# Optimization experiments

Measured on AMD Instinct MI355X. Metric: run time of the kernel, lower is better.

Reference implementation:

```python
import jax, jax.numpy as jnp
from jax import lax
import numpy as np

T, B, NIN, H, NOUT = 256, 64, 512, 512, 512


def _lstm_dir(x, w_ih, w_hh, b_ih, b_hh, reverse):
    # x: [T,B,NIN]; w_ih: [4H,NIN]; w_hh: [4H,H]
    xg = jnp.einsum('tbi,gi->tbg', x, w_ih) + b_ih + b_hh  # [T,B,4H]
    if reverse:
        xg = xg[::-1]
    h0 = jnp.zeros((x.shape[1], w_hh.shape[1]), x.dtype)

    def step(carry, g):
        h, c = carry
        g = g + h @ w_hh.T
        i, f, gg, o = jnp.split(g, 4, axis=-1)  # PyTorch gate order i,f,g,o
        i = jax.nn.sigmoid(i)
        f = jax.nn.sigmoid(f)
        gg = jnp.tanh(gg)
        o = jax.nn.sigmoid(o)
        c = f * c + i * gg
        h = o * jnp.tanh(c)
        return (h, c), h

    _, hs = lax.scan(step, (h0, h0), xg)
    if reverse:
        hs = hs[::-1]
    return hs  # [T,B,H]


def setup_inputs() -> dict:
    key = jax.random.key(0)
    ks = jax.random.split(key, 12)
    s_in = 1.0 / np.sqrt(H)
    u = lambda k, shape: jax.random.uniform(k, shape, jnp.float32, -s_in, s_in)
    return {
        'x': jax.random.normal(ks[0], (T, B, NIN), jnp.float32),
        'w_ih_f': u(ks[1], (4 * H, NIN)),
        'w_hh_f': u(ks[2], (4 * H, H)),
        'b_ih_f': u(ks[3], (4 * H,)),
        'b_hh_f': u(ks[4], (4 * H,)),
        'w_ih_b': u(ks[5], (4 * H, NIN)),
        'w_hh_b': u(ks[6], (4 * H, H)),
        'b_ih_b': u(ks[7], (4 * H,)),
        'b_hh_b': u(ks[8], (4 * H,)),
        'fc_w': u(ks[9], (NOUT, 2 * H)),
        'fc_b': u(ks[10], (NOUT,)),
    }


def reference(x, w_ih_f, w_hh_f, b_ih_f, b_hh_f, w_ih_b, w_hh_b, b_ih_b, b_hh_b, fc_w, fc_b):
    h_f = _lstm_dir(x, w_ih_f, w_hh_f, b_ih_f, b_hh_f, reverse=False)
    h_b = _lstm_dir(x, w_ih_b, w_hh_b, b_ih_b, b_hh_b, reverse=True)
    h = jnp.concatenate([h_f, h_b], axis=-1)  # [T,B,2H]
    out = jnp.einsum('tbh,oh->tbo', h, fc_w) + fc_b  # fused linear over T*B rows
    return out
```

## Files before the change

kernel.cpp:

```cpp
#include <hip/hip_runtime.h>

typedef unsigned short u16;
typedef short v8s __attribute__((ext_vector_type(8)));
typedef float v4f __attribute__((ext_vector_type(4)));

#define TT 256
#define BB 64
#define HH 512
#define G4 2048
#define MTB 16384

static __device__ __forceinline__ float bf2f(u16 u) {
    unsigned int x = ((unsigned int)u) << 16;
    union { unsigned int i; float f; } c; c.i = x; return c.f;
}
static __device__ __forceinline__ u16 f2bf(float f) {
    union { float f; unsigned int i; } c; c.f = f;
    unsigned int u = c.i;
    u += 0x7fffu + ((u >> 16) & 1u);
    return (u16)(u >> 16);
}

__global__ __launch_bounds__(256) void cvt_bf16(const float* __restrict__ src,
                                                u16* __restrict__ dst, int n) {
    int i = blockIdx.x * blockDim.x + threadIdx.x;
    int stride = gridDim.x * blockDim.x;
    for (int j = i * 4; j < n; j += stride * 4) {
        float4 v = *reinterpret_cast<const float4*>(src + j);
        ushort4 o;
        o.x = f2bf(v.x); o.y = f2bf(v.y); o.z = f2bf(v.z); o.w = f2bf(v.w);
        *reinterpret_cast<ushort4*>(dst + j) = o;
    }
}

template<bool OUT_BF16, bool BIAS_M>
__global__ __launch_bounds__(256) void gemm_bt(const u16* __restrict__ A,
                                               const u16* __restrict__ Bm,
                                               void* __restrict__ Cv,
                                               const float* __restrict__ bias1,
                                               const float* __restrict__ bias2,
                                               int M, int N, int K) {
    __shared__ u16 lds_a[128 * 64];
    __shared__ u16 lds_b[128 * 64];
    const int tid = threadIdx.x, lane = tid & 63;
    const int m0 = blockIdx.y * 128, n0 = blockIdx.x * 128;
    const int wid = tid >> 6, wm = wid >> 1, wn = wid & 1;
    v4f acc[4][4] = {};

    const int srow  = tid >> 3;
    const int skoff = (tid & 7) * 8;
    const u16* Ag = A + (size_t)(m0 + srow) * K + skoff;
    const u16* Bg = Bm + (size_t)(n0 + srow) * K + skoff;
    u16* la = lds_a + srow * 64 + skoff;
    u16* lb = lds_b + srow * 64 + skoff;

    for (int k0 = 0; k0 < K; k0 += 64) {
        #pragma unroll
        for (int q = 0; q < 4; ++q) {
            *reinterpret_cast<v8s*>(la + q * 32 * 64) =
                *reinterpret_cast<const v8s*>(Ag + (size_t)q * 32 * K + k0);
            *reinterpret_cast<v8s*>(lb + q * 32 * 64) =
                *reinterpret_cast<const v8s*>(Bg + (size_t)q * 32 * K + k0);
        }
        __syncthreads();
        #pragma unroll
        for (int kk = 0; kk < 2; ++kk) {
            v8s af[4], bfr[4];
            #pragma unroll
            for (int i = 0; i < 4; ++i)
                af[i] = *reinterpret_cast<const v8s*>(
                    lds_a + (wm * 64 + i * 16 + (lane & 15)) * 64 + kk * 32 + (lane >> 4) * 8);
            #pragma unroll
            for (int i = 0; i < 4; ++i)
                bfr[i] = *reinterpret_cast<const v8s*>(
                    lds_b + (wn * 64 + i * 16 + (lane & 15)) * 64 + kk * 32 + (lane >> 4) * 8);
            #pragma unroll
            for (int i = 0; i < 4; ++i)
                #pragma unroll
                for (int j = 0; j < 4; ++j)
                    acc[i][j] = __builtin_amdgcn_mfma_f32_16x16x32_bf16(af[i], bfr[j], acc[i][j], 0, 0, 0);
        }
        __syncthreads();
    }
    #pragma unroll
    for (int i = 0; i < 4; ++i) {
        #pragma unroll
        for (int j = 0; j < 4; ++j) {
            #pragma unroll
            for (int r = 0; r < 4; ++r) {
                int m = m0 + wm * 64 + i * 16 + (lane >> 4) * 4 + r;
                int n = n0 + wn * 64 + j * 16 + (lane & 15);
                float v = acc[i][j][r];
                if (BIAS_M) { v += bias1[m]; if (bias2) v += bias2[m]; }
                else        { v += bias1[n]; }
                if (OUT_BF16) ((u16*)Cv)[(size_t)m * N + n] = f2bf(v);
                else          ((float*)Cv)[(size_t)m * N + n] = v;
            }
        }
    }
}

static __device__ __forceinline__ float sigm(float x) { return 1.f / (1.f + __expf(-x)); }
static __device__ __forceinline__ float tanh_(float x) { return 2.f / (1.f + __expf(-2.f * x)) - 1.f; }

__global__ __launch_bounds__(512, 1) void lstm_persist(
    const u16* __restrict__ w_hh,
    const u16* __restrict__ xgT,
    u16* __restrict__ h_all,
    unsigned* __restrict__ bar)
{
    __shared__ v4f redbuf[16 * 64];
    const int bx = blockIdx.x;
    const int d = bx >> 5, cg = bx & 31;
    const int tid = threadIdx.x;
    const int lane = tid & 63;
    const int nf = (tid >> 6) & 3, kh = tid >> 8;
    const int lrow = lane & 15, lk = lane >> 4;
    const int b = nf * 16 + lrow;

    v8s a[4][8];
    #pragma unroll
    for (int G = 0; G < 4; ++G) {
        const u16* wrow = w_hh + ((size_t)d * G4 + G * HH + cg * 16 + lrow) * HH
                        + kh * 256 + lk * 8;
        #pragma unroll
        for (int q = 0; q < 8; ++q)
            a[G][q] = *reinterpret_cast<const v8s*>(wrow + q * 32);
    }

    float c[4] = {0.f, 0.f, 0.f, 0.f};
    float xg[4][4];
    unsigned* cnt = bar + d * 64;

    {
        const int t0 = d ? (TT - 1) : 0;
        if (kh == 0) {
            const u16* xgb = xgT + (size_t)d * G4 * MTB + (size_t)t0 * BB + b;
            #pragma unroll
            for (int G = 0; G < 4; ++G)
                #pragma unroll
                for (int r = 0; r < 4; ++r)
                    xg[G][r] = bf2f(xgb[(size_t)(G * HH + cg * 16 + lk * 4 + r) * MTB]);
        }
    }

    for (int s = 0; s < TT; ++s) {
        const int t = d ? (TT - 1 - s) : s;

        float xgn[4][4];
        const bool pf = (kh == 0) && (s + 1 < TT);
        if (pf) {
            const int tn = d ? (TT - 2 - s) : (s + 1);
            const u16* xgb = xgT + (size_t)d * G4 * MTB + (size_t)tn * BB + b;
            #pragma unroll
            for (int G = 0; G < 4; ++G)
                #pragma unroll
                for (int r = 0; r < 4; ++r)
                    xgn[G][r] = bf2f(xgb[(size_t)(G * HH + cg * 16 + lk * 4 + r) * MTB]);
        }

        v4f acc[4] = {};
        if (s > 0) {
            const int tprev = d ? (t + 1) : (t - 1);
            const u16* hp = h_all + ((size_t)tprev * BB + b) * 1024 + d * HH
                          + kh * 256 + lk * 8;
            #pragma unroll
            for (int q = 0; q < 8; ++q) {
                union { unsigned long long w[2]; v8s v; } u;
                const u16* p = hp + q * 32;
                u.w[0] = __hip_atomic_load((const unsigned long long*)p,
                                           __ATOMIC_RELAXED, __HIP_MEMORY_SCOPE_AGENT);
                u.w[1] = __hip_atomic_load((const unsigned long long*)(p + 4),
                                           __ATOMIC_RELAXED, __HIP_MEMORY_SCOPE_AGENT);
                #pragma unroll
                for (int G = 0; G < 4; ++G)
                    acc[G] = __builtin_amdgcn_mfma_f32_16x16x32_bf16(a[G][q], u.v, acc[G], 0, 0, 0);
            }
            if (kh == 1) {
                #pragma unroll
                for (int G = 0; G < 4; ++G)
                    redbuf[(nf * 4 + G) * 64 + lane] = acc[G];
            }
        }
        __syncthreads();
        if (kh == 0) {
            ushort4 hout;
            #pragma unroll
            for (int G = 0; G < 4; ++G)
                if (s > 0) acc[G] += redbuf[(nf * 4 + G) * 64 + lane];
            #pragma unroll
            for (int r = 0; r < 4; ++r) {
                float pi = acc[0][r] + xg[0][r];
                float pfv = acc[1][r] + xg[1][r];
                float pg = acc[2][r] + xg[2][r];
                float po = acc[3][r] + xg[3][r];
                float iv = sigm(pi), fv = sigm(pfv), gv = tanh_(pg), ov = sigm(po);
                float cc = fv * c[r] + iv * gv;
                c[r] = cc;
                ((u16*)&hout)[r] = f2bf(ov * tanh_(cc));
            }
            union { ushort4 v; unsigned long long q; } hu; hu.v = hout;
            unsigned long long* hptr = (unsigned long long*)(
                h_all + ((size_t)t * BB + b) * 1024 + d * HH + cg * 16 + lk * 4);
            __hip_atomic_store(hptr, hu.q, __ATOMIC_RELAXED, __HIP_MEMORY_SCOPE_AGENT);
            if (pf) {
                #pragma unroll
                for (int G = 0; G < 4; ++G)
                    #pragma unroll
                    for (int r = 0; r < 4; ++r)
                        xg[G][r] = xgn[G][r];
            }
        }
        __syncthreads();
        if (tid == 0) {
            __hip_atomic_fetch_add(cnt, 1u, __ATOMIC_RELAXED, __HIP_MEMORY_SCOPE_AGENT);
            const unsigned target = 32u * (unsigned)(s + 1);
            while (__hip_atomic_load(cnt, __ATOMIC_RELAXED, __HIP_MEMORY_SCOPE_AGENT) < target)
                __builtin_amdgcn_s_sleep(1);
        }
        __syncthreads();
    }
}

extern "C" void kernel_launch(void* const* d_in, const int* in_sizes, int n_in,
                              void* d_out, int out_size, void* d_ws, size_t ws_size,
                              hipStream_t stream) {
    const float* x    = (const float*)d_in[0];
    const float* wihf = (const float*)d_in[1];
    const float* whhf = (const float*)d_in[2];
    const float* bihf = (const float*)d_in[3];
    const float* bhhf = (const float*)d_in[4];
    const float* wihb = (const float*)d_in[5];
    const float* whhb = (const float*)d_in[6];
    const float* bihb = (const float*)d_in[7];
    const float* bhhb = (const float*)d_in[8];
    const float* fcw  = (const float*)d_in[9];
    const float* fcb  = (const float*)d_in[10];

    char* ws = (char*)d_ws;
    size_t off = 0;
    auto alloc = [&](size_t bytes) {
        off = (off + 255) & ~(size_t)255;
        char* p = ws + off; off += bytes; return p;
    };
    u16* x_bf    = (u16*)alloc((size_t)MTB * 512 * 2);
    u16* wih_bf  = (u16*)alloc((size_t)2 * G4 * 512 * 2);
    u16* whh_bf  = (u16*)alloc((size_t)2 * G4 * 512 * 2);
    u16* fcw_bf  = (u16*)alloc((size_t)512 * 1024 * 2);
    u16* xgT     = (u16*)alloc((size_t)2 * G4 * MTB * 2);
    u16* h_all   = (u16*)alloc((size_t)MTB * 1024 * 2);
    unsigned* bar = (unsigned*)alloc(512);
    (void)ws_size;

    cvt_bf16<<<1024, 256, 0, stream>>>(x, x_bf, MTB * 512);
    cvt_bf16<<<256, 256, 0, stream>>>(wihf, wih_bf, G4 * 512);
    cvt_bf16<<<256, 256, 0, stream>>>(wihb, wih_bf + (size_t)G4 * 512, G4 * 512);
    cvt_bf16<<<256, 256, 0, stream>>>(whhf, whh_bf, G4 * 512);
    cvt_bf16<<<256, 256, 0, stream>>>(whhb, whh_bf + (size_t)G4 * 512, G4 * 512);
    cvt_bf16<<<128, 256, 0, stream>>>(fcw, fcw_bf, 512 * 1024);

    gemm_bt<true, true><<<dim3(MTB / 128, G4 / 128), 256, 0, stream>>>(
        wih_bf, x_bf, xgT, bihf, bhhf, G4, MTB, 512);
    gemm_bt<true, true><<<dim3(MTB / 128, G4 / 128), 256, 0, stream>>>(
        wih_bf + (size_t)G4 * 512, x_bf, xgT + (size_t)G4 * MTB, bihb, bhhb, G4, MTB, 512);

    hipMemsetAsync(bar, 0, 512, stream);
    lstm_persist<<<64, 512, 0, stream>>>(whh_bf, xgT, h_all, bar);

    gemm_bt<false, false><<<dim3(512 / 128, MTB / 128), 256, 0, stream>>>(
        h_all, fcw_bf, d_out, fcb, nullptr, MTB, 512, 1024);
}
```

Measured before the change: 1.697 ms.

## Replace block-wide barrier with per-wave flag sync in persistent LSTM kernel

Restructures the recurrent kernel so each wave owns one batch slice and covers the full K=512 reduction itself, holding 64 weight fragments in registers. This removes the split-K shared-memory reduction and both __syncthreads per step. The global atomic counter barrier becomes per-(direction, batch-slice) flags that each wave polls with a wave-wide vote, so only waves that depend on each other synchronize. The cost is higher register pressure, twice the serial MFMA chain per wave, fewer threads per block, and reliance on relaxed atomics plus a vmcnt wait for ordering.

```diff
diff --git a/kernel.cpp b/kernel.cpp
--- a/kernel.cpp
+++ b/kernel.cpp
@@ -103,122 +103,106 @@
 static __device__ __forceinline__ float sigm(float x) { return 1.f / (1.f + __expf(-x)); }
 static __device__ __forceinline__ float tanh_(float x) { return 2.f / (1.f + __expf(-2.f * x)) - 1.f; }
 
-__global__ __launch_bounds__(512, 1) void lstm_persist(
+__global__ __launch_bounds__(256, 1) void lstm_persist(
     const u16* __restrict__ w_hh,
     const u16* __restrict__ xgT,
     u16* __restrict__ h_all,
-    unsigned* __restrict__ bar)
+    unsigned* __restrict__ flags)
 {
-    __shared__ v4f redbuf[16 * 64];
     const int bx = blockIdx.x;
     const int d = bx >> 5, cg = bx & 31;
-    const int tid = threadIdx.x;
-    const int lane = tid & 63;
-    const int nf = (tid >> 6) & 3, kh = tid >> 8;
+    const int lane = threadIdx.x & 63, nf = threadIdx.x >> 6;
     const int lrow = lane & 15, lk = lane >> 4;
     const int b = nf * 16 + lrow;
 
-    v8s a[4][8];
+    v8s a[4][16];
     #pragma unroll
     for (int G = 0; G < 4; ++G) {
-        const u16* wrow = w_hh + ((size_t)d * G4 + G * HH + cg * 16 + lrow) * HH
-                        + kh * 256 + lk * 8;
-        #pragma unroll
-        for (int q = 0; q < 8; ++q)
-            a[G][q] = *reinterpret_cast<const v8s*>(wrow + q * 32);
-    }
+        const u16* wrow = w_hh + ((size_t)d * G4 + G * HH + cg * 16 + lrow) * HH + lk * 8;
+        #pragma unroll
+        for (int kk = 0; kk < 16; ++kk)
+            a[G][kk] = *reinterpret_cast<const v8s*>(wrow + kk * 32);
+    }
+    #pragma unroll
+    for (int G = 0; G < 4; ++G)
+        #pragma unroll
+        for (int kk = 0; kk < 16; ++kk)
+            asm volatile("" : "+v"(a[G][kk]));
 
     float c[4] = {0.f, 0.f, 0.f, 0.f};
     float xg[4][4];
-    unsigned* cnt = bar + d * 64;
+    unsigned* fl = flags + (d * 4 + nf) * 32;
 
     {
         const int t0 = d ? (TT - 1) : 0;
-        if (kh == 0) {
-            const u16* xgb = xgT + (size_t)d * G4 * MTB + (size_t)t0 * BB + b;
+        const u16* xgb = xgT + (size_t)d * G4 * MTB + (size_t)t0 * BB + b;
+        #pragma unroll
+        for (int G = 0; G < 4; ++G)
+            #pragma unroll
+            for (int r = 0; r < 4; ++r)
+                xg[G][r] = bf2f(xgb[(size_t)(G * HH + cg * 16 + lk * 4 + r) * MTB]);
+    }
+
+    for (int s = 0; s < TT; ++s) {
+        const int t = d ? (TT - 1 - s) : s;
+        v4f acc[4] = {};
+        if (s > 0) {
+            const unsigned tgt = (unsigned)s;
+            while (true) {
+                unsigned fv = __hip_atomic_load(&fl[lane & 31],
+                                                __ATOMIC_RELAXED, __HIP_MEMORY_SCOPE_AGENT);
+                if (__all((int)(fv >= tgt))) break;
+                __builtin_amdgcn_s_sleep(2);
+            }
+            asm volatile("" ::: "memory");
+            const int tprev = d ? (t + 1) : (t - 1);
+            const u16* hp = h_all + ((size_t)tprev * BB + b) * 1024 + d * HH + lk * 8;
+            v8s bf_[16];
+            #pragma unroll
+            for (int kk = 0; kk < 16; ++kk) {
+                union { unsigned long long w[2]; v8s v; } u;
+                const u16* p = hp + kk * 32;
+                u.w[0] = __hip_atomic_load((const unsigned long long*)p,
+                                           __ATOMIC_RELAXED, __HIP_MEMORY_SCOPE_AGENT);
+                u.w[1] = __hip_atomic_load((const unsigned long long*)(p + 4),
+                                           __ATOMIC_RELAXED, __HIP_MEMORY_SCOPE_AGENT);
+                bf_[kk] = u.v;
+            }
+            #pragma unroll
+            for (int kk = 0; kk < 16; ++kk)
+                #pragma unroll
+                for (int G = 0; G < 4; ++G)
+                    acc[G] = __builtin_amdgcn_mfma_f32_16x16x32_bf16(a[G][kk], bf_[kk], acc[G], 0, 0, 0);
+        }
+        ushort4 hout;
+        #pragma unroll
+        for (int r = 0; r < 4; ++r) {
+            float pi = acc[0][r] + xg[0][r];
+            float pf = acc[1][r] + xg[1][r];
+            float pg = acc[2][r] + xg[2][r];
+            float po = acc[3][r] + xg[3][r];
+            float iv = sigm(pi), fv = sigm(pf), gv = tanh_(pg), ov = sigm(po);
+            float cc = fv * c[r] + iv * gv;
+            c[r] = cc;
+            ((u16*)&hout)[r] = f2bf(ov * tanh_(cc));
+        }
+        union { ushort4 v; unsigned long long q; } hu; hu.v = hout;
+        __hip_atomic_store((unsigned long long*)(
+                h_all + ((size_t)t * BB + b) * 1024 + d * HH + cg * 16 + lk * 4),
+            hu.q, __ATOMIC_RELAXED, __HIP_MEMORY_SCOPE_AGENT);
+        asm volatile("s_waitcnt vmcnt(0)" ::: "memory");
+        if (lane == 0)
+            __hip_atomic_store(&fl[cg], (unsigned)(s + 1),
+                               __ATOMIC_RELAXED, __HIP_MEMORY_SCOPE_AGENT);
+        if (s + 1 < TT) {
+            const int tn = d ? (TT - 2 - s) : (s + 1);
+            const u16* xgb = xgT + (size_t)d * G4 * MTB + (size_t)tn * BB + b;
             #pragma unroll
             for (int G = 0; G < 4; ++G)
                 #pragma unroll
                 for (int r = 0; r < 4; ++r)
                     xg[G][r] = bf2f(xgb[(size_t)(G * HH + cg * 16 + lk * 4 + r) * MTB]);
         }
-    }
-
-    for (int s = 0; s < TT; ++s) {
-        const int t = d ? (TT - 1 - s) : s;
-
-        float xgn[4][4];
-        const bool pf = (kh == 0) && (s + 1 < TT);
-        if (pf) {
-            const int tn = d ? (TT - 2 - s) : (s + 1);
-            const u16* xgb = xgT + (size_t)d * G4 * MTB + (size_t)tn * BB + b;
-            #pragma unroll
-            for (int G = 0; G < 4; ++G)
-                #pragma unroll
-                for (int r = 0; r < 4; ++r)
-                    xgn[G][r] = bf2f(xgb[(size_t)(G * HH + cg * 16 + lk * 4 + r) * MTB]);
-        }
-
-        v4f acc[4] = {};
-        if (s > 0) {
-            const int tprev = d ? (t + 1) : (t - 1);
-            const u16* hp = h_all + ((size_t)tprev * BB + b) * 1024 + d * HH
-                          + kh * 256 + lk * 8;
-            #pragma unroll
-            for (int q = 0; q < 8; ++q) {
-                union { unsigned long long w[2]; v8s v; } u;
-                const u16* p = hp + q * 32;
-                u.w[0] = __hip_atomic_load((const unsigned long long*)p,
-                                           __ATOMIC_RELAXED, __HIP_MEMORY_SCOPE_AGENT);
-                u.w[1] = __hip_atomic_load((const unsigned long long*)(p + 4),
-                                           __ATOMIC_RELAXED, __HIP_MEMORY_SCOPE_AGENT);
-                #pragma unroll
-                for (int G = 0; G < 4; ++G)
-                    acc[G] = __builtin_amdgcn_mfma_f32_16x16x32_bf16(a[G][q], u.v, acc[G], 0, 0, 0);
-            }
-            if (kh == 1) {
-                #pragma unroll
-                for (int G = 0; G < 4; ++G)
-                    redbuf[(nf * 4 + G) * 64 + lane] = acc[G];
-            }
-        }
-        __syncthreads();
-        if (kh == 0) {
-            ushort4 hout;
-            #pragma unroll
-            for (int G = 0; G < 4; ++G)
-                if (s > 0) acc[G] += redbuf[(nf * 4 + G) * 64 + lane];
-            #pragma unroll
-            for (int r = 0; r < 4; ++r) {
-                float pi = acc[0][r] + xg[0][r];
-                float pfv = acc[1][r] + xg[1][r];
-                float pg = acc[2][r] + xg[2][r];
-                float po = acc[3][r] + xg[3][r];
-                float iv = sigm(pi), fv = sigm(pfv), gv = tanh_(pg), ov = sigm(po);
-                float cc = fv * c[r] + iv * gv;
-                c[r] = cc;
-                ((u16*)&hout)[r] = f2bf(ov * tanh_(cc));
-            }
-            union { ushort4 v; unsigned long long q; } hu; hu.v = hout;
-            unsigned long long* hptr = (unsigned long long*)(
-                h_all + ((size_t)t * BB + b) * 1024 + d * HH + cg * 16 + lk * 4);
-            __hip_atomic_store(hptr, hu.q, __ATOMIC_RELAXED, __HIP_MEMORY_SCOPE_AGENT);
-            if (pf) {
-                #pragma unroll
-                for (int G = 0; G < 4; ++G)
-                    #pragma unroll
-                    for (int r = 0; r < 4; ++r)
-                        xg[G][r] = xgn[G][r];
-            }
-        }
-        __syncthreads();
-        if (tid == 0) {
-            __hip_atomic_fetch_add(cnt, 1u, __ATOMIC_RELAXED, __HIP_MEMORY_SCOPE_AGENT);
-            const unsigned target = 32u * (unsigned)(s + 1);
-            while (__hip_atomic_load(cnt, __ATOMIC_RELAXED, __HIP_MEMORY_SCOPE_AGENT) < target)
-                __builtin_amdgcn_s_sleep(1);
-        }
-        __syncthreads();
     }
 }
 
@@ -249,7 +233,7 @@
     u16* fcw_bf  = (u16*)alloc((size_t)512 * 1024 * 2);
     u16* xgT     = (u16*)alloc((size_t)2 * G4 * MTB * 2);
     u16* h_all   = (u16*)alloc((size_t)MTB * 1024 * 2);
-    unsigned* bar = (unsigned*)alloc(512);
+    unsigned* flags = (unsigned*)alloc(2 * 4 * 32 * sizeof(unsigned));
     (void)ws_size;
 
     cvt_bf16<<<1024, 256, 0, stream>>>(x, x_bf, MTB * 512);
@@ -264,8 +248,8 @@
     gemm_bt<true, true><<<dim3(MTB / 128, G4 / 128), 256, 0, stream>>>(
         wih_bf + (size_t)G4 * 512, x_bf, xgT + (size_t)G4 * MTB, bihb, bhhb, G4, MTB, 512);
 
-    hipMemsetAsync(bar, 0, 512, stream);
-    lstm_persist<<<64, 512, 0, stream>>>(whh_bf, xgT, h_all, bar);
+    hipMemsetAsync(flags, 0, 2 * 4 * 32 * sizeof(unsigned), stream);
+    lstm_persist<<<64, 256, 0, stream>>>(whh_bf, xgT, h_all, flags);
 
     gemm_bt<false, false><<<dim3(512 / 128, MTB / 128), 256, 0, stream>>>(
         h_all, fcw_bf, d_out, fcb, nullptr, MTB, 512, 1024);
```

Result: slower. 2.291 ms (+35.0%).
